# Optimization experiments

Hardware: AMD Instinct MI355X
Metric: run time of the kernel (lower is better)

The kernel has to match this reference:

```python
import math
import jax, jax.numpy as jnp
import numpy as np

HEADS = 9
EMBED = 32
TEMPERATURE = 3000.0

def _conv1x1(x, W, b):
    # x: [B,C,H,W], W: [O,C], b: [O]  (1x1 conv == channel matmul)
    return jnp.einsum('bchw,oc->bohw', x, W) + b[None, :, None, None]

def setup_inputs() -> dict:
    key = jax.random.key(0)
    ks = jax.random.split(key, 14)
    B, H, W = 2, 64, 64
    h2, w2 = 32, 32
    hd = HEADS * EMBED  # 288
    s = 0.1
    return {
        'second_frame': jax.random.normal(ks[0], (B, 3, H, W), jnp.float32),
        'first_frame_aligned': jax.random.normal(ks[1], (B, 3, H, W), jnp.float32),
        'second_frame_feat': jax.random.normal(ks[2], (B, 4, h2, w2), jnp.float32),
        'first_frame_feat_aligned': jax.random.normal(ks[3], (B, 4, h2, w2), jnp.float32),
        'Wq': jax.random.normal(ks[4], (hd, 3), jnp.float32) * s,
        'bq': jax.random.normal(ks[5], (hd,), jnp.float32) * s,
        'Wk': jax.random.normal(ks[6], (hd, 3), jnp.float32) * s,
        'bk': jax.random.normal(ks[7], (hd,), jnp.float32) * s,
        'Wv': jax.random.normal(ks[8], (hd, 4), jnp.float32) * s,
        'bv': jax.random.normal(ks[9], (hd,), jnp.float32) * s,
        'Wp': jax.random.normal(ks[10], (4, hd), jnp.float32) * s,
        'bp': jax.random.normal(ks[11], (4,), jnp.float32) * s,
        'Wt': jax.random.normal(ks[12], (1, EMBED), jnp.float32) * s,
        'bt': jax.random.normal(ks[13], (1,), jnp.float32) * s,
    }

def reference(second_frame, first_frame_aligned, second_frame_feat,
              first_frame_feat_aligned, Wq, bq, Wk, bk, Wv, bv, Wp, bp, Wt, bt):
    B, _, H, W = second_frame.shape
    HW = H * W
    # bilinear upsample of aligned features to (H, W); half-pixel centers == align_corners=False
    feat_up = jax.image.resize(first_frame_feat_aligned,
                               (B, first_frame_feat_aligned.shape[1], H, W),
                               method='linear', antialias=False)
    Q = _conv1x1(second_frame, Wq, bq).reshape(B, HEADS, EMBED, HW)
    K = _conv1x1(first_frame_aligned, Wk, bk).reshape(B, HEADS, EMBED, HW)
    V = _conv1x1(feat_up, Wv, bv).reshape(B, HEADS, EMBED, HW)
    Qn = jnp.transpose(Q, (0, 1, 3, 2))                      # [B,h,HW,d]
    sim = jnp.einsum('bhnd,bhdm->bhnm', Qn, K) / math.sqrt(EMBED)  # [B,h,HW,HW]
    # learned per-query threshold from Q
    t = jnp.einsum('bhnd,od->bhno', Qn, Wt) + bt             # [B,h,HW,1]
    attn = jax.nn.relu((sim - t) / TEMPERATURE)              # no row normalization
    out = jnp.einsum('bhnm,bhdm->bhnd', attn, V)             # [B,h,HW,d]
    out = jnp.transpose(out, (0, 1, 3, 2)).reshape(B, HEADS * EMBED, H, W)
    out_feat = _conv1x1(out, Wp, bp)                         # [B,4,H,W]
    h2, w2 = second_frame_feat.shape[-2:]
    out_feat_down = jax.image.resize(out_feat, (B, out_feat.shape[1], h2, w2),
                                     method='linear', antialias=False)
    final_feat = second_frame_feat + out_feat_down
    return final_feat, out_feat_down
```

## Files before the change

### kernel.cpp

```cpp
#include <hip/hip_runtime.h>
#include <hip/hip_bf16.h>
#include <cstddef>

#define NHEADS 9
#define D 32
#define SQ 4096
#define ZSPLIT 8
#define MBLK (SQ / ZSPLIT)
#define NSTEPS (MBLK / 32)

typedef __attribute__((ext_vector_type(8))) short bf16x8;
typedef __attribute__((ext_vector_type(4))) float f32x4;

__device__ __forceinline__ unsigned int f2bf(float f) {
    unsigned int u = __float_as_uint(f);
    u += 0x7fffu + ((u >> 16) & 1u);
    return u >> 16;
}

__device__ __forceinline__ unsigned int trunc_pk(float lo, float hi) {
    return __builtin_amdgcn_perm(__float_as_uint(hi), __float_as_uint(lo),
                                 0x07060302u);
}

__device__ __forceinline__ bf16x8 relu_pack8(f32x4 s1, f32x4 s2) {
    union { unsigned int u[4]; bf16x8 v; } P;
    P.u[0] = trunc_pk(s1[0], s1[1]);
    P.u[1] = trunc_pk(s1[2], s1[3]);
    P.u[2] = trunc_pk(s2[0], s2[1]);
    P.u[3] = trunc_pk(s2[2], s2[3]);
    const bf16x8 z = {0, 0, 0, 0, 0, 0, 0, 0};
    return __builtin_elementwise_max(P.v, z);
}

__global__ __launch_bounds__(256) void prep_kernel(
    const float* __restrict__ x2, const float* __restrict__ x1,
    const float* __restrict__ feat1,
    const float* __restrict__ Wq, const float* __restrict__ bq,
    const float* __restrict__ Wk, const float* __restrict__ bk,
    const float* __restrict__ Wv, const float* __restrict__ bv,
    const float* __restrict__ Wt, const float* __restrict__ bt,
    unsigned short* __restrict__ Qb, unsigned short* __restrict__ Kb,
    unsigned short* __restrict__ Vt, float* __restrict__ tbuf)
{
    __shared__ unsigned short Vls[32 * 66];

    const int tid = threadIdx.x;
    int idx = blockIdx.x * blockDim.x + tid;
    int g  = idx & 3;
    int nl = tid >> 2;
    int n  = (idx >> 2) & (SQ - 1);
    int bh = idx >> 14;
    int h  = bh % NHEADS;
    int b  = bh / NHEADS;

    float xs0 = x2[((size_t)b * 3 + 0) * SQ + n];
    float xs1 = x2[((size_t)b * 3 + 1) * SQ + n];
    float xs2 = x2[((size_t)b * 3 + 2) * SQ + n];
    float ys0 = x1[((size_t)b * 3 + 0) * SQ + n];
    float ys1 = x1[((size_t)b * 3 + 1) * SQ + n];
    float ys2 = x1[((size_t)b * 3 + 2) * SQ + n];

    int yy = n >> 6, xx = n & 63;
    int jy = yy >> 1, jx = xx >> 1;
    int j0, j1, i0, i1; float wy0, wy1, wx0, wx1;
    if (yy & 1) { j0 = jy; j1 = (jy < 31) ? jy + 1 : 31; wy0 = 0.75f; wy1 = 0.25f; }
    else        { j0 = (jy > 0) ? jy - 1 : 0; j1 = jy;   wy0 = 0.25f; wy1 = 0.75f; }
    if (xx & 1) { i0 = jx; i1 = (jx < 31) ? jx + 1 : 31; wx0 = 0.75f; wx1 = 0.25f; }
    else        { i0 = (jx > 0) ? jx - 1 : 0; i1 = jx;   wx0 = 0.25f; wx1 = 0.75f; }

    float fu[4];
#pragma unroll
    for (int c = 0; c < 4; ++c) {
        const float* f = feat1 + ((size_t)b * 4 + c) * 1024;
        fu[c] = wy0 * (wx0 * f[j0 * 32 + i0] + wx1 * f[j0 * 32 + i1]) +
                wy1 * (wx0 * f[j1 * 32 + i0] + wx1 * f[j1 * 32 + i1]);
    }

    const int d0 = g * 8;
    unsigned int qp[4], kp[4];
    float tpart = 0.0f;
#pragma unroll
    for (int j = 0; j < 8; ++j) {
        int d = d0 + j, hd = h * D + d;
        float q = bq[hd] + Wq[hd * 3] * xs0 + Wq[hd * 3 + 1] * xs1 + Wq[hd * 3 + 2] * xs2;
        float k = bk[hd] + Wk[hd * 3] * ys0 + Wk[hd * 3 + 1] * ys1 + Wk[hd * 3 + 2] * ys2;
        float v = bv[hd] + Wv[hd * 4] * fu[0] + Wv[hd * 4 + 1] * fu[1] +
                  Wv[hd * 4 + 2] * fu[2] + Wv[hd * 4 + 3] * fu[3];
        tpart += q * Wt[d];
        unsigned int qb_ = f2bf(q), kb_ = f2bf(k);
        if (j & 1) { qp[j >> 1] |= qb_ << 16; kp[j >> 1] |= kb_ << 16; }
        else       { qp[j >> 1]  = qb_;       kp[j >> 1]  = kb_; }
        Vls[d * 66 + nl] = (unsigned short)f2bf(v);
    }
    tpart += __shfl_xor(tpart, 1);
    tpart += __shfl_xor(tpart, 2);
    if (g == 0) tbuf[(size_t)bh * SQ + n] = tpart + bt[0];

    *(uint4*)(Qb + ((size_t)bh * SQ + n) * D + d0) =
        make_uint4(qp[0], qp[1], qp[2], qp[3]);

    {
        int nl_  = n & 63;
        int slot = (nl_ & 32) + 4 * ((nl_ >> 3) & 3) + (nl_ & 3) + ((nl_ & 4) << 2);
        size_t kaddr = ((size_t)bh * SQ + (n & ~63) + slot) * D + d0;
        *(uint4*)(Kb + kaddr) = make_uint4(kp[0], kp[1], kp[2], kp[3]);
    }

    __syncthreads();
    {
        int r  = tid >> 3;
        int c4 = tid & 7;
        int n0 = (blockIdx.x & 63) * 64;
        unsigned int w0 = *(const unsigned int*)&Vls[r * 66 + c4 * 4];
        unsigned int w1 = *(const unsigned int*)&Vls[r * 66 + c4 * 4 + 2];
        *(uint2*)(Vt + ((size_t)bh * D + r) * SQ + n0 + c4 * 4) = make_uint2(w0, w1);
    }
}

#define STEP_LOAD(S, K1, K2, VL, VH)                                           \
    K1 = *(const bf16x8*)(kbase + (size_t)(S) * (32 * D));                     \
    K2 = *(const bf16x8*)(kbase + (size_t)(S) * (32 * D) + 16 * D);            \
    VL = *(const bf16x8*)(vbase + (S) * 32);                                   \
    VH = *(const bf16x8*)(vbase + (S) * 32 + 16 * SQ);

#define STEP_COMPUTE(K1, K2, VL, VH)                                           \
    {                                                                          \
        f32x4 sA1 = __builtin_amdgcn_mfma_f32_16x16x32_bf16(K1, qfA, ciA, 0, 0, 0);\
        f32x4 sA2 = __builtin_amdgcn_mfma_f32_16x16x32_bf16(K2, qfA, ciA, 0, 0, 0);\
        f32x4 sB1 = __builtin_amdgcn_mfma_f32_16x16x32_bf16(K1, qfB, ciB, 0, 0, 0);\
        f32x4 sB2 = __builtin_amdgcn_mfma_f32_16x16x32_bf16(K2, qfB, ciB, 0, 0, 0);\
        f32x4 sC1 = __builtin_amdgcn_mfma_f32_16x16x32_bf16(K1, qfC, ciC, 0, 0, 0);\
        f32x4 sC2 = __builtin_amdgcn_mfma_f32_16x16x32_bf16(K2, qfC, ciC, 0, 0, 0);\
        f32x4 sD1 = __builtin_amdgcn_mfma_f32_16x16x32_bf16(K1, qfD, ciD, 0, 0, 0);\
        f32x4 sD2 = __builtin_amdgcn_mfma_f32_16x16x32_bf16(K2, qfD, ciD, 0, 0, 0);\
        bf16x8 pA = relu_pack8(sA1, sA2);                                      \
        bf16x8 pB = relu_pack8(sB1, sB2);                                      \
        bf16x8 pC = relu_pack8(sC1, sC2);                                      \
        bf16x8 pD = relu_pack8(sD1, sD2);                                      \
        accAl = __builtin_amdgcn_mfma_f32_16x16x32_bf16(VL, pA, accAl, 0, 0, 0);\
        accAh = __builtin_amdgcn_mfma_f32_16x16x32_bf16(VH, pA, accAh, 0, 0, 0);\
        accBl = __builtin_amdgcn_mfma_f32_16x16x32_bf16(VL, pB, accBl, 0, 0, 0);\
        accBh = __builtin_amdgcn_mfma_f32_16x16x32_bf16(VH, pB, accBh, 0, 0, 0);\
        accCl = __builtin_amdgcn_mfma_f32_16x16x32_bf16(VL, pC, accCl, 0, 0, 0);\
        accCh = __builtin_amdgcn_mfma_f32_16x16x32_bf16(VH, pC, accCh, 0, 0, 0);\
        accDl = __builtin_amdgcn_mfma_f32_16x16x32_bf16(VL, pD, accDl, 0, 0, 0);\
        accDh = __builtin_amdgcn_mfma_f32_16x16x32_bf16(VH, pD, accDh, 0, 0, 0);\
    }

__global__ __launch_bounds__(256, 4) void attn_kernel(
    const unsigned short* __restrict__ Qb,
    const unsigned short* __restrict__ Kb,
    const unsigned short* __restrict__ Vt,
    const float* __restrict__ tbuf,
    const float* __restrict__ Wp,
    float* __restrict__ ofp)
{
    const int lin  = blockIdx.x;
    const int xcd  = lin & 7;
    const int q8   = lin >> 3;
    const int xblk = q8 & 15;
    const int gl   = q8 >> 4;
    const int grp  = xcd * 18 + gl;
    const int bh   = grp >> 3;
    const int zz   = grp & 7;
    const int h    = bh % NHEADS;
    const int n0   = xblk * 256;
    const int mc0  = zz * MBLK;
    const int tid  = threadIdx.x;
    const int wave = tid >> 6;
    const int lane = tid & 63;
    const int l15  = lane & 15;
    const int quad = lane >> 4;

    const int nw = n0 + wave * 64;

    const unsigned short* qbase = Qb + ((size_t)bh * SQ + nw + l15) * D + quad * 8;
    bf16x8 qfA = *(const bf16x8*)(qbase);
    bf16x8 qfB = *(const bf16x8*)(qbase + 16 * D);
    bf16x8 qfC = *(const bf16x8*)(qbase + 32 * D);
    bf16x8 qfD = *(const bf16x8*)(qbase + 48 * D);

    const float SQRT32 = 5.656854249492381f;
    const float* tb = tbuf + (size_t)bh * SQ + nw + l15;
    float TA = tb[0]  * SQRT32;
    float TB = tb[16] * SQRT32;
    float TC = tb[32] * SQRT32;
    float TD = tb[48] * SQRT32;
    const f32x4 ciA = {-TA, -TA, -TA, -TA};
    const f32x4 ciB = {-TB, -TB, -TB, -TB};
    const f32x4 ciC = {-TC, -TC, -TC, -TC};
    const f32x4 ciD = {-TD, -TD, -TD, -TD};

    const unsigned short* kbase = Kb + ((size_t)bh * SQ + mc0 + l15) * D + quad * 8;
    const unsigned short* vbase = Vt + ((size_t)bh * D + l15) * SQ + mc0 + quad * 8;

    f32x4 accAl = {0.f,0.f,0.f,0.f}, accAh = {0.f,0.f,0.f,0.f};
    f32x4 accBl = {0.f,0.f,0.f,0.f}, accBh = {0.f,0.f,0.f,0.f};
    f32x4 accCl = {0.f,0.f,0.f,0.f}, accCh = {0.f,0.f,0.f,0.f};
    f32x4 accDl = {0.f,0.f,0.f,0.f}, accDh = {0.f,0.f,0.f,0.f};

    bf16x8 k1a, k2a, vla, vha, k1b, k2b, vlb, vhb;
    STEP_LOAD(0, k1a, k2a, vla, vha);
#pragma unroll
    for (int s = 0; s < NSTEPS; s += 2) {
        STEP_LOAD(s + 1, k1b, k2b, vlb, vhb);
        STEP_COMPUTE(k1a, k2a, vla, vha);
        {
            const int na = (s + 2 < NSTEPS) ? s + 2 : NSTEPS - 1;
            STEP_LOAD(na, k1a, k2a, vla, vha);
        }
        STEP_COMPUTE(k1b, k2b, vlb, vhb);
    }

    const float s1 = 5.892556509887896e-05f;
    const float* wph = Wp + h * D + quad * 4;
    float* obase = ofp + ((size_t)(bh * 8 + zz) * 4) * SQ + nw + l15;
#pragma unroll
    for (int o = 0; o < 4; ++o) {
        float cA = 0.f, cB = 0.f, cC = 0.f, cD = 0.f;
#pragma unroll
        for (int r = 0; r < 4; ++r) {
            float wlo = wph[o * 288 + r], whi = wph[o * 288 + 16 + r];
            cA += accAl[r] * wlo + accAh[r] * whi;
            cB += accBl[r] * wlo + accBh[r] * whi;
            cC += accCl[r] * wlo + accCh[r] * whi;
            cD += accDl[r] * wlo + accDh[r] * whi;
        }
        cA += __shfl_xor(cA, 16); cA += __shfl_xor(cA, 32);
        cB += __shfl_xor(cB, 16); cB += __shfl_xor(cB, 32);
        cC += __shfl_xor(cC, 16); cC += __shfl_xor(cC, 32);
        cD += __shfl_xor(cD, 16); cD += __shfl_xor(cD, 32);
        if (quad == 0) {
            float* ob = obase + (size_t)o * SQ;
            ob[0]  = cA * s1;
            ob[16] = cB * s1;
            ob[32] = cC * s1;
            ob[48] = cD * s1;
        }
    }
}

__global__ __launch_bounds__(256) void final_kernel(
    const float* __restrict__ ofp,
    const float* __restrict__ sff,
    const float* __restrict__ bp,
    float* __restrict__ dout)
{
    int t = blockIdx.x * 256 + threadIdx.x;
    int out = t >> 3;
    int s   = t & 7;
    int i  = out & 31;
    int jj = (out >> 5) & 31;
    int bo = out >> 10;
    int o  = bo & 3;
    int b  = bo >> 2;
    int nbase = (jj * 2) * 64 + i * 2;

    float acc = 0.0f;
#pragma unroll
    for (int h = 0; h < NHEADS; ++h) {
        const float* src = ofp +
            ((size_t)(((b * NHEADS + h) * 8 + s) * 4 + o)) * SQ + nbase;
        acc += src[0] + src[1] + src[64] + src[65];
    }
    acc += __shfl_xor(acc, 1);
    acc += __shfl_xor(acc, 2);
    acc += __shfl_xor(acc, 4);
    if (s == 0) {
        float dval = 0.25f * acc + bp[o];
        dout[out]        = sff[out] + dval;
        dout[8192 + out] = dval;
    }
}

extern "C" void kernel_launch(void* const* d_in, const int* in_sizes, int n_in,
                              void* d_out, int out_size, void* d_ws, size_t ws_size,
                              hipStream_t stream)
{
    const float* second_frame = (const float*)d_in[0];
    const float* first_frame  = (const float*)d_in[1];
    const float* sff          = (const float*)d_in[2];
    const float* ffa          = (const float*)d_in[3];
    const float* Wq = (const float*)d_in[4];
    const float* bq = (const float*)d_in[5];
    const float* Wk = (const float*)d_in[6];
    const float* bk = (const float*)d_in[7];
    const float* Wv = (const float*)d_in[8];
    const float* bv = (const float*)d_in[9];
    const float* Wp = (const float*)d_in[10];
    const float* bp = (const float*)d_in[11];
    const float* Wt = (const float*)d_in[12];
    const float* bt = (const float*)d_in[13];
    float* out = (float*)d_out;

    char* ws = (char*)d_ws;
    const size_t QKV = (size_t)2 * NHEADS * SQ * D * sizeof(unsigned short);
    unsigned short* Qb = (unsigned short*)ws;
    unsigned short* Kb = (unsigned short*)(ws + QKV);
    unsigned short* Vt = (unsigned short*)(ws + 2 * QKV);
    float* tbuf = (float*)(ws + 3 * QKV);
    float* ofp  = (float*)(ws + 3 * QKV + (size_t)2 * NHEADS * SQ * sizeof(float));

    prep_kernel<<<1152, 256, 0, stream>>>(second_frame, first_frame, ffa,
                                          Wq, bq, Wk, bk, Wv, bv, Wt, bt,
                                          Qb, Kb, Vt, tbuf);
    attn_kernel<<<16 * 18 * ZSPLIT, 256, 0, stream>>>(Qb, Kb, Vt, tbuf, Wp, ofp);
    final_kernel<<<256, 256, 0, stream>>>(ofp, sff, bp, out);
}
```

Baseline: 162.9 us.

## Tile V into per-step fragment layout and triple-buffer K/V loads

The projection kernel now writes V in a blocked layout where each 32-key step is a contiguous 1024-element tile, ordered so every lane reads one 16-byte fragment. This replaces strided per-row reads across the full sequence length. The attention loop is also fully unrolled with three register buffers, so loads run two steps ahead of compute instead of one. The cost is more registers per thread, which may pressure the occupancy target of 4 blocks per SM.

```diff
diff --git a/kernel.cpp b/kernel.cpp
--- a/kernel.cpp
+++ b/kernel.cpp
@@ -109,20 +109,24 @@
 
     __syncthreads();
     {
-        int r  = tid >> 3;
-        int c4 = tid & 7;
-        int n0 = (blockIdx.x & 63) * 64;
-        unsigned int w0 = *(const unsigned int*)&Vls[r * 66 + c4 * 4];
-        unsigned int w1 = *(const unsigned int*)&Vls[r * 66 + c4 * 4 + 2];
-        *(uint2*)(Vt + ((size_t)bh * D + r) * SQ + n0 + c4 * 4) = make_uint2(w0, w1);
+        int r   = tid >> 3;
+        int c4  = tid & 7;
+        int blk = blockIdx.x & 63;
+        unsigned int w0 = *(const unsigned int*)&Vls[r * 66 + c4 * 8];
+        unsigned int w1 = *(const unsigned int*)&Vls[r * 66 + c4 * 8 + 2];
+        unsigned int w2 = *(const unsigned int*)&Vls[r * 66 + c4 * 8 + 4];
+        unsigned int w3 = *(const unsigned int*)&Vls[r * 66 + c4 * 8 + 6];
+        size_t dst = ((size_t)bh * 128 + blk * 2 + (c4 >> 2)) * 1024
+                   + (r >> 4) * 512 + (c4 & 3) * 128 + (r & 15) * 8;
+        *(uint4*)(Vt + dst) = make_uint4(w0, w1, w2, w3);
     }
 }
 
 #define STEP_LOAD(S, K1, K2, VL, VH)                                           \
     K1 = *(const bf16x8*)(kbase + (size_t)(S) * (32 * D));                     \
     K2 = *(const bf16x8*)(kbase + (size_t)(S) * (32 * D) + 16 * D);            \
-    VL = *(const bf16x8*)(vbase + (S) * 32);                                   \
-    VH = *(const bf16x8*)(vbase + (S) * 32 + 16 * SQ);
+    VL = *(const bf16x8*)(vbase + (size_t)(S) * 1024);                         \
+    VH = *(const bf16x8*)(vbase + (size_t)(S) * 1024 + 512);
 
 #define STEP_COMPUTE(K1, K2, VL, VH)                                           \
     {                                                                          \
@@ -147,6 +151,10 @@
         accDl = __builtin_amdgcn_mfma_f32_16x16x32_bf16(VL, pD, accDl, 0, 0, 0);\
         accDh = __builtin_amdgcn_mfma_f32_16x16x32_bf16(VH, pD, accDh, 0, 0, 0);\
     }
+
+#define PIPE(SL, KL1, KL2, VLL, VLH, KC1, KC2, VCL, VCH)                       \
+    STEP_LOAD(SL, KL1, KL2, VLL, VLH);                                         \
+    STEP_COMPUTE(KC1, KC2, VCL, VCH);
 
 __global__ __launch_bounds__(256, 4) void attn_kernel(
     const unsigned short* __restrict__ Qb,
@@ -193,25 +201,32 @@
     const f32x4 ciD = {-TD, -TD, -TD, -TD};
 
     const unsigned short* kbase = Kb + ((size_t)bh * SQ + mc0 + l15) * D + quad * 8;
-    const unsigned short* vbase = Vt + ((size_t)bh * D + l15) * SQ + mc0 + quad * 8;
+    const unsigned short* vbase = Vt + ((size_t)bh * 128 + (mc0 >> 5)) * 1024 + lane * 8;
 
     f32x4 accAl = {0.f,0.f,0.f,0.f}, accAh = {0.f,0.f,0.f,0.f};
     f32x4 accBl = {0.f,0.f,0.f,0.f}, accBh = {0.f,0.f,0.f,0.f};
     f32x4 accCl = {0.f,0.f,0.f,0.f}, accCh = {0.f,0.f,0.f,0.f};
     f32x4 accDl = {0.f,0.f,0.f,0.f}, accDh = {0.f,0.f,0.f,0.f};
 
-    bf16x8 k1a, k2a, vla, vha, k1b, k2b, vlb, vhb;
+    bf16x8 k1a,k2a,vla,vha, k1b,k2b,vlb,vhb, k1c,k2c,vlc,vhc;
     STEP_LOAD(0, k1a, k2a, vla, vha);
-#pragma unroll
-    for (int s = 0; s < NSTEPS; s += 2) {
-        STEP_LOAD(s + 1, k1b, k2b, vlb, vhb);
-        STEP_COMPUTE(k1a, k2a, vla, vha);
-        {
-            const int na = (s + 2 < NSTEPS) ? s + 2 : NSTEPS - 1;
-            STEP_LOAD(na, k1a, k2a, vla, vha);
-        }
-        STEP_COMPUTE(k1b, k2b, vlb, vhb);
-    }
+    STEP_LOAD(1, k1b, k2b, vlb, vhb);
+    PIPE( 2, k1c,k2c,vlc,vhc, k1a,k2a,vla,vha)
+    PIPE( 3, k1a,k2a,vla,vha, k1b,k2b,vlb,vhb)
+    PIPE( 4, k1b,k2b,vlb,vhb, k1c,k2c,vlc,vhc)
+    PIPE( 5, k1c,k2c,vlc,vhc, k1a,k2a,vla,vha)
+    PIPE( 6, k1a,k2a,vla,vha, k1b,k2b,vlb,vhb)
+    PIPE( 7, k1b,k2b,vlb,vhb, k1c,k2c,vlc,vhc)
+    PIPE( 8, k1c,k2c,vlc,vhc, k1a,k2a,vla,vha)
+    PIPE( 9, k1a,k2a,vla,vha, k1b,k2b,vlb,vhb)
+    PIPE(10, k1b,k2b,vlb,vhb, k1c,k2c,vlc,vhc)
+    PIPE(11, k1c,k2c,vlc,vhc, k1a,k2a,vla,vha)
+    PIPE(12, k1a,k2a,vla,vha, k1b,k2b,vlb,vhb)
+    PIPE(13, k1b,k2b,vlb,vhb, k1c,k2c,vlc,vhc)
+    PIPE(14, k1c,k2c,vlc,vhc, k1a,k2a,vla,vha)
+    PIPE(15, k1a,k2a,vla,vha, k1b,k2b,vlb,vhb)
+    STEP_COMPUTE(k1c, k2c, vlc, vhc);
+    STEP_COMPUTE(k1a, k2a, vla, vha);
 
     const float s1 = 5.892556509887896e-05f;
     const float* wph = Wp + h * D + quad * 4;
```

Result: faster. 142.3 us (-12.6%).

## Stage K/V tiles through LDS with async global_load_lds triple buffering

Applied to the files above, without the earlier changes.

The attention kernel now copies K and V chunks of 64 keys into a three-slot shared-memory ring with direct global-to-LDS loads. Each chunk is loaded once per block and shared by all four waves, where before each wave loaded its own K/V fragments straight from global memory. The prep kernel writes V in a new tiled layout so that each chunk is a contiguous 2048-element block that can be copied linearly. This cuts redundant global traffic but adds a block-wide barrier every chunk plus LDS reads, and the last chunk is issued redundantly.

```diff
diff --git a/kernel.cpp b/kernel.cpp
--- a/kernel.cpp
+++ b/kernel.cpp
@@ -7,7 +7,7 @@
 #define SQ 4096
 #define ZSPLIT 8
 #define MBLK (SQ / ZSPLIT)
-#define NSTEPS (MBLK / 32)
+#define CHUNKS (MBLK / 64)
 
 typedef __attribute__((ext_vector_type(8))) short bf16x8;
 typedef __attribute__((ext_vector_type(4))) float f32x4;
@@ -31,6 +31,13 @@
     P.u[3] = trunc_pk(s2[2], s2[3]);
     const bf16x8 z = {0, 0, 0, 0, 0, 0, 0, 0};
     return __builtin_elementwise_max(P.v, z);
+}
+
+__device__ __forceinline__ void gload_lds16(const unsigned short* g,
+                                            unsigned short* l) {
+    __builtin_amdgcn_global_load_lds(
+        (const __attribute__((address_space(1))) unsigned int*)g,
+        (__attribute__((address_space(3))) unsigned int*)l, 16, 0, 0);
 }
 
 __global__ __launch_bounds__(256) void prep_kernel(
@@ -109,20 +116,18 @@
 
     __syncthreads();
     {
-        int r  = tid >> 3;
-        int c4 = tid & 7;
-        int n0 = (blockIdx.x & 63) * 64;
-        unsigned int w0 = *(const unsigned int*)&Vls[r * 66 + c4 * 4];
-        unsigned int w1 = *(const unsigned int*)&Vls[r * 66 + c4 * 4 + 2];
-        *(uint2*)(Vt + ((size_t)bh * D + r) * SQ + n0 + c4 * 4) = make_uint2(w0, w1);
-    }
-}
-
-#define STEP_LOAD(S, K1, K2, VL, VH)                                           \
-    K1 = *(const bf16x8*)(kbase + (size_t)(S) * (32 * D));                     \
-    K2 = *(const bf16x8*)(kbase + (size_t)(S) * (32 * D) + 16 * D);            \
-    VL = *(const bf16x8*)(vbase + (S) * 32);                                   \
-    VH = *(const bf16x8*)(vbase + (S) * 32 + 16 * SQ);
+        int r   = tid >> 3;
+        int c4  = tid & 7;
+        int blk = blockIdx.x & 63;
+        unsigned int w0 = *(const unsigned int*)&Vls[r * 66 + c4 * 8];
+        unsigned int w1 = *(const unsigned int*)&Vls[r * 66 + c4 * 8 + 2];
+        unsigned int w2 = *(const unsigned int*)&Vls[r * 66 + c4 * 8 + 4];
+        unsigned int w3 = *(const unsigned int*)&Vls[r * 66 + c4 * 8 + 6];
+        size_t dst = ((size_t)bh * 128 + blk * 2 + (c4 >> 2)) * 1024
+                   + (r >> 4) * 512 + (c4 & 3) * 128 + (r & 15) * 8;
+        *(uint4*)(Vt + dst) = make_uint4(w0, w1, w2, w3);
+    }
+}
 
 #define STEP_COMPUTE(K1, K2, VL, VH)                                           \
     {                                                                          \
@@ -156,6 +161,9 @@
     const float* __restrict__ Wp,
     float* __restrict__ ofp)
 {
+    __shared__ __align__(16) unsigned short Kls[3][2048];
+    __shared__ __align__(16) unsigned short Vls3[3][2048];
+
     const int lin  = blockIdx.x;
     const int xcd  = lin & 7;
     const int q8   = lin >> 3;
@@ -192,26 +200,52 @@
     const f32x4 ciC = {-TC, -TC, -TC, -TC};
     const f32x4 ciD = {-TD, -TD, -TD, -TD};
 
-    const unsigned short* kbase = Kb + ((size_t)bh * SQ + mc0 + l15) * D + quad * 8;
-    const unsigned short* vbase = Vt + ((size_t)bh * D + l15) * SQ + mc0 + quad * 8;
+    const unsigned short* Kg = Kb + ((size_t)bh * SQ + mc0) * D + tid * 8;
+    const unsigned short* Vg = Vt + ((size_t)bh * 128 + (mc0 >> 5)) * 1024 + tid * 8;
+    const int wv = wave * 512;
+
+    const int koff = l15 * 32 + quad * 8;
+    const int voff = lane * 8;
+
+#define ISSUE(C, S)                                                            \
+    gload_lds16(Kg + (size_t)(C) * 2048, &Kls[S][wv]);                         \
+    gload_lds16(Vg + (size_t)(C) * 2048, &Vls3[S][wv]);
+
+#define CCHUNK(S)                                                              \
+    {                                                                          \
+        const unsigned short* Kp = &Kls[S][0];                                 \
+        const unsigned short* Vp = &Vls3[S][0];                                \
+        bf16x8 k1 = *(const bf16x8*)(Kp + koff);                               \
+        bf16x8 k2 = *(const bf16x8*)(Kp + 512 + koff);                         \
+        bf16x8 vl = *(const bf16x8*)(Vp + voff);                               \
+        bf16x8 vh = *(const bf16x8*)(Vp + 512 + voff);                         \
+        STEP_COMPUTE(k1, k2, vl, vh);                                          \
+        k1 = *(const bf16x8*)(Kp + 1024 + koff);                               \
+        k2 = *(const bf16x8*)(Kp + 1536 + koff);                               \
+        vl = *(const bf16x8*)(Vp + 1024 + voff);                               \
+        vh = *(const bf16x8*)(Vp + 1536 + voff);                               \
+        STEP_COMPUTE(k1, k2, vl, vh);                                          \
+    }
 
     f32x4 accAl = {0.f,0.f,0.f,0.f}, accAh = {0.f,0.f,0.f,0.f};
     f32x4 accBl = {0.f,0.f,0.f,0.f}, accBh = {0.f,0.f,0.f,0.f};
     f32x4 accCl = {0.f,0.f,0.f,0.f}, accCh = {0.f,0.f,0.f,0.f};
     f32x4 accDl = {0.f,0.f,0.f,0.f}, accDh = {0.f,0.f,0.f,0.f};
 
-    bf16x8 k1a, k2a, vla, vha, k1b, k2b, vlb, vhb;
-    STEP_LOAD(0, k1a, k2a, vla, vha);
-#pragma unroll
-    for (int s = 0; s < NSTEPS; s += 2) {
-        STEP_LOAD(s + 1, k1b, k2b, vlb, vhb);
-        STEP_COMPUTE(k1a, k2a, vla, vha);
+    ISSUE(0, 0);
+    ISSUE(1, 1);
+
+#pragma unroll
+    for (int c = 0; c < CHUNKS; ++c) {
+        asm volatile("s_waitcnt vmcnt(2)" ::: "memory");
+        __builtin_amdgcn_s_barrier();
         {
-            const int na = (s + 2 < NSTEPS) ? s + 2 : NSTEPS - 1;
-            STEP_LOAD(na, k1a, k2a, vla, vha);
+            const int nc = (c + 2 < CHUNKS) ? c + 2 : CHUNKS - 1;
+            ISSUE(nc, (c + 2) % 3);
         }
-        STEP_COMPUTE(k1b, k2b, vlb, vhb);
-    }
+        CCHUNK(c % 3);
+    }
+    asm volatile("s_waitcnt vmcnt(0)" ::: "memory");
 
     const float s1 = 5.892556509887896e-05f;
     const float* wph = Wp + h * D + quad * 4;
```

Result: faster. 134.8 us (-17.2%).
